# Performance work log

Measured on AMD Instinct MI355X. Metric: run time of the kernel, lower is better.

Reference implementation:

```python
import jax, jax.numpy as jnp
import numpy as np

N_USERS = 100_000
N_ITEMS = 50_000
N_NODES = N_USERS + N_ITEMS
D = 64
NUM_LAYERS = 3
N_INTER = 1_000_000  # interactions; symmetrized -> 2M directed edges
BATCH = 4096


def setup_inputs() -> dict:
    key = jax.random.key(0)
    k_u, k_i, k_r, k_c, k_uid, k_iid = jax.random.split(key, 6)
    user_embedding = jax.random.normal(k_u, (N_USERS, D), dtype=jnp.float32)
    item_embedding = jax.random.normal(k_i, (N_ITEMS, D), dtype=jnp.float32)

    # build symmetric normalized adjacency edges as in get_norm_adj_mat
    rng = np.random.default_rng(0)
    row = rng.integers(0, N_USERS, size=N_INTER)
    col = rng.integers(0, N_ITEMS, size=N_INTER) + N_USERS
    src = np.concatenate([row, col])
    dst = np.concatenate([col, row])
    deg = np.bincount(src, minlength=N_NODES).astype(np.float32)
    norm_deg = 1.0 / np.sqrt(np.where(deg == 0, 1.0, deg))
    edge_weight = (norm_deg[src] * norm_deg[dst]).astype(np.float32)
    edge_index = np.stack([src, dst]).astype(np.int64)

    user_id = jax.random.randint(k_uid, (BATCH,), 0, N_USERS)
    item_id = jax.random.randint(k_iid, (BATCH,), 0, N_ITEMS)
    return {
        "user_embedding": user_embedding,
        "item_embedding": item_embedding,
        "edge_weight": jnp.asarray(edge_weight),
        "edge_index": jnp.asarray(edge_index),
        "user_id": user_id,
        "item_id": item_id,
    }


def reference(user_embedding, item_embedding, edge_weight, edge_index, user_id, item_id):
    # ego embeddings: [N_NODES, D]
    x = jnp.concatenate([user_embedding, item_embedding], axis=0)
    src, dst = edge_index[0], edge_index[1]
    h = x
    acc = x  # running sum over layer outputs (incl. layer 0)
    for _ in range(NUM_LAYERS):
        # LightGCNConv: gather source, scale by edge weight, scatter-add to dest
        msg = h[src] * edge_weight[:, None]                       # [E, D]
        h = jax.ops.segment_sum(msg, dst, num_segments=N_NODES)   # [N, D]
        acc = acc + h
    final = acc / jnp.asarray(NUM_LAYERS + 1, dtype=x.dtype)      # mean over layers
    u_embed = final[:N_USERS][user_id]
    i_embed = final[N_USERS:][item_id]
    return (u_embed, i_embed)
```

## Files before the change

### kernel.cpp

```cpp
#include <hip/hip_runtime.h>

#define N_USERS 100000
#define N_NODES 150000
#define DIM 64
#define BATCH 4096
#define BSHIFT 8
#define BUCKET 256
#define NB 586
#define NBP 768
#define PAIRS_PER_BLK 2048
#define STRIP 4096
#define CAPSHIFT 13
#define CAP (1 << CAPSHIFT)

typedef unsigned short bf16_t;

static __device__ __forceinline__ float bf2f(bf16_t h) {
    return __uint_as_float(((unsigned)h) << 16);
}
static __device__ __forceinline__ bf16_t f2bf(float f) {
    unsigned u = __float_as_uint(f);
    return (bf16_t)((u + 0x7FFFu + ((u >> 16) & 1u)) >> 16);
}

__global__ void __launch_bounds__(256)
lgcn_bin(const int* __restrict__ row, const int* __restrict__ col,
         int* __restrict__ pos, int* __restrict__ binned, int EH) {
    __shared__ int cnt[NBP];
    __shared__ int sA[256], sB[256];
    __shared__ int base[NB + 2];
    __shared__ int stage[STRIP];
    int tid = threadIdx.x;
    int k = blockIdx.x;
    cnt[tid] = 0; cnt[tid + 256] = 0; cnt[tid + 512] = 0;
    __syncthreads();
    int e0 = k * PAIRS_PER_BLK;
    int e1 = min(EH, e0 + PAIRS_PER_BLK);
    int n = e1 - e0;
    int nq = n >> 2;
    const int4* r4 = (const int4*)(row + e0);
    const int4* c4 = (const int4*)(col + e0);
    for (int q = tid; q < nq; q += 256) {
        int4 r = r4[q]; int4 c = c4[q];
        atomicAdd(&cnt[r.x >> BSHIFT], 1); atomicAdd(&cnt[c.x >> BSHIFT], 1);
        atomicAdd(&cnt[r.y >> BSHIFT], 1); atomicAdd(&cnt[c.y >> BSHIFT], 1);
        atomicAdd(&cnt[r.z >> BSHIFT], 1); atomicAdd(&cnt[c.z >> BSHIFT], 1);
        atomicAdd(&cnt[r.w >> BSHIFT], 1); atomicAdd(&cnt[c.w >> BSHIFT], 1);
    }
    __syncthreads();
    int c0 = cnt[3 * tid], c1 = cnt[3 * tid + 1], c2 = cnt[3 * tid + 2];
    int s = c0 + c1 + c2;
    sA[tid] = s;
    __syncthreads();
    int* c_ = sA; int* n_ = sB;
    for (int off = 1; off < 256; off <<= 1) {
        n_[tid] = (tid >= off) ? c_[tid] + c_[tid - off] : c_[tid];
        __syncthreads();
        int* t = c_; c_ = n_; n_ = t;
    }
    int excl = c_[tid] - s;
    if (3 * tid     <= NB) base[3 * tid]     = excl;
    if (3 * tid + 1 <= NB) base[3 * tid + 1] = excl + c0;
    if (3 * tid + 2 <= NB) base[3 * tid + 2] = excl + c0 + c1;
    __syncthreads();
    for (int i = tid; i <= NB; i += 256) {
        pos[k * (NB + 1) + i] = base[i];
        cnt[i] = base[i];
    }
    __syncthreads();
    for (int q = tid; q < nq; q += 256) {
        int4 r = r4[q]; int4 c = c4[q];
        int rr[4] = { r.x, r.y, r.z, r.w };
        int cc[4] = { c.x, c.y, c.z, c.w };
#pragma unroll
        for (int j = 0; j < 4; ++j) {
            int p1 = atomicAdd(&cnt[cc[j] >> BSHIFT], 1);
            stage[p1] = ((cc[j] & (BUCKET - 1)) << 18) | rr[j];
            int p2 = atomicAdd(&cnt[rr[j] >> BSHIFT], 1);
            stage[p2] = ((rr[j] & (BUCKET - 1)) << 18) | cc[j];
        }
    }
    __syncthreads();
    int m4 = (2 * n) >> 2;
    int4* dst = (int4*)(binned + k * STRIP);
    const int4* st4 = (const int4*)stage;
    for (int j = tid; j < m4; j += 256) dst[j] = st4[j];
}

__global__ void __launch_bounds__(256)
lgcn_build_csr(const int* __restrict__ pos, const int* __restrict__ binned,
               int4* __restrict__ nodeinfo, int* __restrict__ packed,
               const float* __restrict__ ue, const float* __restrict__ ie,
               bf16_t* __restrict__ g0, bf16_t* __restrict__ g1, int nblk) {
    __shared__ int stage[CAP];
    __shared__ int sA[256], sB[256];
    __shared__ int hist[256], cur[256];
    int b = blockIdx.x;
    int tid = threadIdx.x;
    int gb = b << CAPSHIFT;
    int a0 = 0, l0 = 0, a1 = 0, l1 = 0;
    if (tid < nblk) {
        const int* pk = pos + tid * (NB + 1) + b;
        a0 = pk[0]; l0 = pk[1] - a0;
    }
    if (tid + 256 < nblk) {
        const int* pk = pos + (tid + 256) * (NB + 1) + b;
        a1 = pk[0]; l1 = pk[1] - a1;
    }
    int u = l0 + l1;
    sA[tid] = u;
    __syncthreads();
    int* c_ = sA; int* n_ = sB;
    for (int off = 1; off < 256; off <<= 1) {
        n_[tid] = (tid >= off) ? c_[tid] + c_[tid - off] : c_[tid];
        __syncthreads();
        int* t = c_; c_ = n_; n_ = t;
    }
    int myBase = c_[tid] - u;
    int Eb = c_[255];
    __syncthreads();
    {
        const int* s0 = binned + tid * STRIP + a0;
        int i = 0;
        for (; i + 4 <= l0; i += 4) {
            int w0 = s0[i], w1 = s0[i + 1], w2 = s0[i + 2], w3 = s0[i + 3];
            stage[myBase + i] = w0;     stage[myBase + i + 1] = w1;
            stage[myBase + i + 2] = w2; stage[myBase + i + 3] = w3;
        }
        for (; i < l0; ++i) stage[myBase + i] = s0[i];
        const int* s1 = binned + (tid + 256) * STRIP + a1;
        int bb = myBase + l0;
        i = 0;
        for (; i + 4 <= l1; i += 4) {
            int w0 = s1[i], w1 = s1[i + 1], w2 = s1[i + 2], w3 = s1[i + 3];
            stage[bb + i] = w0;     stage[bb + i + 1] = w1;
            stage[bb + i + 2] = w2; stage[bb + i + 3] = w3;
        }
        for (; i < l1; ++i) stage[bb + i] = s1[i];
    }
    hist[tid] = 0;
    __syncthreads();
    for (int j = tid; j < Eb; j += 256)
        atomicAdd(&hist[stage[j] >> 18], 1);
    __syncthreads();
    int deg = hist[tid];
    int degp = (deg + 3) & ~3;
    sA[tid] = degp;
    __syncthreads();
    int* c2 = sA; int* n2 = sB;
    for (int off = 1; off < 256; off <<= 1) {
        n2[tid] = (tid >= off) ? c2[tid] + c2[tid - off] : c2[tid];
        __syncthreads();
        int* t = c2; c2 = n2; n2 = t;
    }
    int startLoc = c2[tid] - degp;
    cur[tid] = startLoc;
    int node = (b << BSHIFT) + tid;
    float da = (deg == 0) ? 1.0f : (float)deg;
    float sq = sqrtf(da);
    float nm = 1.0f / sq;
    if (node < N_NODES) {
        int4 ni;
        ni.x = gb + startLoc;
        ni.y = deg;
        ni.z = __float_as_int(nm);
        ni.w = __float_as_int(sq);
        nodeinfo[node] = ni;
    }
    __syncthreads();
    hist[tid] = __float_as_int(nm);
    for (int kk = deg; kk < degp; ++kk)
        packed[gb + startLoc + kk] = N_NODES;
    for (int j = tid; j < Eb; j += 256) {
        int w = stage[j];
        int p = atomicAdd(&cur[w >> 18], 1);
        packed[gb + p] = w & 0x3FFFF;
    }
    int firstNode = b << BSHIFT;
    int nloc = min(BUCKET, N_NODES - firstNode);
    const int nU16 = N_USERS * (DIM / 4);
    int t0 = firstNode * (DIM / 4);
    for (int i = tid; i < nloc * (DIM / 4); i += 256) {
        int t = t0 + i;
        float4 x = (t < nU16) ? ((const float4*)ue)[t]
                              : ((const float4*)ie)[t - nU16];
        float nrm = __int_as_float(hist[i >> 4]);
        ushort4 o;
        o.x = f2bf(x.x * nrm); o.y = f2bf(x.y * nrm);
        o.z = f2bf(x.z * nrm); o.w = f2bf(x.w * nrm);
        ((ushort4*)g0)[t] = o;
    }
    if (b == 0 && tid < 32) {
        const int nT = N_NODES * (DIM / 4);
        if (tid < 16) ((ushort4*)g0)[nT + tid] = make_ushort4(0, 0, 0, 0);
        else          ((ushort4*)g1)[nT + tid - 16] = make_ushort4(0, 0, 0, 0);
    }
}


static __device__ __forceinline__ float
gather_lane(const bf16_t* __restrict__ g, const int* __restrict__ packed,
            int su, int dp, int lane) {
    float acc = 0.f;
    const int4* p4 = (const int4*)(packed + su);
    int k = 0;
    for (; k + 8 <= dp; k += 8) {
        int4 ea = p4[k >> 2];
        int4 eb = p4[(k >> 2) + 1];
        const bf16_t* r0 = g + ((unsigned)ea.x << 6);
        const bf16_t* r1 = g + ((unsigned)ea.y << 6);
        const bf16_t* r2 = g + ((unsigned)ea.z << 6);
        const bf16_t* r3 = g + ((unsigned)ea.w << 6);
        const bf16_t* r4 = g + ((unsigned)eb.x << 6);
        const bf16_t* r5 = g + ((unsigned)eb.y << 6);
        const bf16_t* r6 = g + ((unsigned)eb.z << 6);
        const bf16_t* r7 = g + ((unsigned)eb.w << 6);
        float v0 = bf2f(r0[lane]); float v1 = bf2f(r1[lane]);
        float v2 = bf2f(r2[lane]); float v3 = bf2f(r3[lane]);
        float v4 = bf2f(r4[lane]); float v5 = bf2f(r5[lane]);
        float v6 = bf2f(r6[lane]); float v7 = bf2f(r7[lane]);
        acc += ((v0 + v1) + (v2 + v3)) + ((v4 + v5) + (v6 + v7));
    }
    if (k < dp) {
        int4 ea = p4[k >> 2];
        const bf16_t* r0 = g + ((unsigned)ea.x << 6);
        const bf16_t* r1 = g + ((unsigned)ea.y << 6);
        const bf16_t* r2 = g + ((unsigned)ea.z << 6);
        const bf16_t* r3 = g + ((unsigned)ea.w << 6);
        float v0 = bf2f(r0[lane]); float v1 = bf2f(r1[lane]);
        float v2 = bf2f(r2[lane]); float v3 = bf2f(r3[lane]);
        acc += (v0 + v1) + (v2 + v3);
    }
    return acc;
}

__global__ void __launch_bounds__(256)
lgcn_pull(const bf16_t* __restrict__ g, const int4* __restrict__ nodeinfo,
          const int* __restrict__ packed, bf16_t* __restrict__ gn) {
    int n = blockIdx.x * 4 + (threadIdx.x >> 6);
    if (n >= N_NODES) return;
    n = __builtin_amdgcn_readfirstlane(n);
    int lane = threadIdx.x & 63;
    int4 ni = nodeinfo[n];
    int su = __builtin_amdgcn_readfirstlane(ni.x);
    int du = __builtin_amdgcn_readfirstlane(ni.y);
    int dp = (du + 3) & ~3;
    float acc = gather_lane(g, packed, su, dp, lane);
    float nm = __int_as_float(ni.z);
    gn[((unsigned)n << 6) + lane] = f2bf(acc * nm * nm);
}

__global__ void __launch_bounds__(256)
lgcn_final(const float* __restrict__ ue, const float* __restrict__ ie,
           const bf16_t* __restrict__ g1, const bf16_t* __restrict__ g2,
           const int4* __restrict__ nodeinfo, const int* __restrict__ packed,
           const int* __restrict__ uid, const int* __restrict__ iid,
           float* __restrict__ out) {
    int slot = blockIdx.x * 4 + (threadIdx.x >> 6);
    if (slot >= 2 * BATCH) return;
    slot = __builtin_amdgcn_readfirstlane(slot);
    int lane = threadIdx.x & 63;
    int isItem = slot >= BATCH;
    int b = isItem ? (slot - BATCH) : slot;
    int node = isItem ? (N_USERS + iid[b]) : uid[b];
    node = __builtin_amdgcn_readfirstlane(node);
    int4 ni = nodeinfo[node];
    int su = __builtin_amdgcn_readfirstlane(ni.x);
    int du = __builtin_amdgcn_readfirstlane(ni.y);
    int dp = (du + 3) & ~3;
    float acc = gather_lane(g2, packed, su, dp, lane);
    const float* xb = isItem ? (ie + ((unsigned)(node - N_USERS) << 6))
                             : (ue + ((unsigned)node << 6));
    float x = xb[lane];
    float a1 = bf2f(g1[((unsigned)node << 6) + lane]);
    float a2 = bf2f(g2[((unsigned)node << 6) + lane]);
    float rn = __int_as_float(ni.w);
    float nm = __int_as_float(ni.z);
    out[((unsigned)slot << 6) + lane] = 0.25f * (x + rn * (a1 + a2) + nm * acc);
}


extern "C" void kernel_launch(void* const* d_in, const int* in_sizes, int n_in,
                              void* d_out, int out_size, void* d_ws, size_t ws_size,
                              hipStream_t stream) {
    const float* ue  = (const float*)d_in[0];
    const float* ie  = (const float*)d_in[1];
    const int*   ei  = (const int*)d_in[3];
    const int*   uid = (const int*)d_in[4];
    const int*   iid = (const int*)d_in[5];
    float* out = (float*)d_out;

    const int E  = in_sizes[2];
    const int EH = E / 2;
    const int* row = ei;
    const int* col = ei + E;

    const int nblk = (EH + PAIRS_PER_BLK - 1) / PAIRS_PER_BLK;

    char* p = (char*)d_ws;
    size_t off = 0;
    auto carve = [&](size_t bytes) -> char* {
        char* r = p + off;
        off += (bytes + 255) & ~(size_t)255;
        return r;
    };
    const size_t nodeBf16 = (size_t)(N_NODES + 1) * DIM * sizeof(bf16_t);
    bf16_t* gA       = (bf16_t*)carve(nodeBf16);
    bf16_t* gB       = (bf16_t*)carve(nodeBf16);
    int4*   nodeinfo = (int4*)carve((size_t)N_NODES * sizeof(int4));
    int*    pos      = (int*)carve((size_t)nblk * (NB + 1) * sizeof(int));
    int*    binned   = (int*)carve((size_t)nblk * STRIP * sizeof(int));
    int*    packed   = (int*)carve((size_t)NB * CAP * sizeof(int));
    (void)ws_size;

    lgcn_bin<<<nblk, 256, 0, stream>>>(row, col, pos, binned, EH);
    lgcn_build_csr<<<NB, 256, 0, stream>>>(pos, binned, nodeinfo, packed,
                                           ue, ie, gA, gB, nblk);
    const int pullGrid = (N_NODES + 3) / 4;
    lgcn_pull<<<pullGrid, 256, 0, stream>>>(gA, nodeinfo, packed, gB);
    lgcn_pull<<<pullGrid, 256, 0, stream>>>(gB, nodeinfo, packed, gA);
    lgcn_final<<<(2 * BATCH + 3) / 4, 256, 0, stream>>>(
        ue, ie, gB, gA, nodeinfo, packed, uid, iid, out);
}
```

Baseline: 225.5 us.

## Fuse propagation layers and final gather into one persistent kernel with grid barriers

Replaces the two pull launches and the final kernel with a single persistent kernel of 2048 blocks. Waves grid-stride over nodes and are separated by atomic-counter grid barriers, and the counter is reset inside the bin kernel. This removes two kernel launch boundaries and their tail drain, at the cost of spin-wait barriers and a fixed grid that must be fully co-resident to avoid deadlock. Static node striding may also balance load worse than one wave per node.

```diff
diff --git a/kernel.cpp b/kernel.cpp
--- a/kernel.cpp
+++ b/kernel.cpp
@@ -12,6 +12,8 @@
 #define STRIP 4096
 #define CAPSHIFT 13
 #define CAP (1 << CAPSHIFT)
+#define PROP_BLOCKS 2048
+#define PROP_WAVES (PROP_BLOCKS * 4)
 
 typedef unsigned short bf16_t;
 
@@ -25,13 +27,15 @@
 
 __global__ void __launch_bounds__(256)
 lgcn_bin(const int* __restrict__ row, const int* __restrict__ col,
-         int* __restrict__ pos, int* __restrict__ binned, int EH) {
+         int* __restrict__ pos, int* __restrict__ binned, int EH,
+         int* __restrict__ bar) {
     __shared__ int cnt[NBP];
     __shared__ int sA[256], sB[256];
     __shared__ int base[NB + 2];
     __shared__ int stage[STRIP];
     int tid = threadIdx.x;
     int k = blockIdx.x;
+    if (k == 0 && tid == 0) bar[0] = 0;
     cnt[tid] = 0; cnt[tid + 256] = 0; cnt[tid + 512] = 0;
     __syncthreads();
     int e0 = k * PAIRS_PER_BLK;
@@ -234,49 +238,73 @@
     return acc;
 }
 
-__global__ void __launch_bounds__(256)
-lgcn_pull(const bf16_t* __restrict__ g, const int4* __restrict__ nodeinfo,
-          const int* __restrict__ packed, bf16_t* __restrict__ gn) {
-    int n = blockIdx.x * 4 + (threadIdx.x >> 6);
-    if (n >= N_NODES) return;
-    n = __builtin_amdgcn_readfirstlane(n);
+static __device__ __forceinline__ void
+grid_barrier(int* bar, int target) {
+    __syncthreads();
+    if (threadIdx.x == 0) {
+        __hip_atomic_fetch_add(bar, 1, __ATOMIC_RELEASE,
+                               __HIP_MEMORY_SCOPE_AGENT);
+        while (__hip_atomic_load(bar, __ATOMIC_RELAXED,
+                                 __HIP_MEMORY_SCOPE_AGENT) < target)
+            __builtin_amdgcn_s_sleep(64);
+        (void)__hip_atomic_load(bar, __ATOMIC_ACQUIRE,
+                                __HIP_MEMORY_SCOPE_AGENT);
+    }
+    __syncthreads();
+}
+
+__global__ void __launch_bounds__(256, 8)
+lgcn_prop(bf16_t* __restrict__ gA, bf16_t* __restrict__ gB,
+          const int4* __restrict__ nodeinfo, const int* __restrict__ packed,
+          const float* __restrict__ ue, const float* __restrict__ ie,
+          const int* __restrict__ uid, const int* __restrict__ iid,
+          float* __restrict__ out, int* bar) {
+    int gw = blockIdx.x * 4 + (threadIdx.x >> 6);
     int lane = threadIdx.x & 63;
-    int4 ni = nodeinfo[n];
-    int su = __builtin_amdgcn_readfirstlane(ni.x);
-    int du = __builtin_amdgcn_readfirstlane(ni.y);
-    int dp = (du + 3) & ~3;
-    float acc = gather_lane(g, packed, su, dp, lane);
-    float nm = __int_as_float(ni.z);
-    gn[((unsigned)n << 6) + lane] = f2bf(acc * nm * nm);
-}
-
-__global__ void __launch_bounds__(256)
-lgcn_final(const float* __restrict__ ue, const float* __restrict__ ie,
-           const bf16_t* __restrict__ g1, const bf16_t* __restrict__ g2,
-           const int4* __restrict__ nodeinfo, const int* __restrict__ packed,
-           const int* __restrict__ uid, const int* __restrict__ iid,
-           float* __restrict__ out) {
-    int slot = blockIdx.x * 4 + (threadIdx.x >> 6);
-    if (slot >= 2 * BATCH) return;
-    slot = __builtin_amdgcn_readfirstlane(slot);
-    int lane = threadIdx.x & 63;
-    int isItem = slot >= BATCH;
-    int b = isItem ? (slot - BATCH) : slot;
-    int node = isItem ? (N_USERS + iid[b]) : uid[b];
-    node = __builtin_amdgcn_readfirstlane(node);
-    int4 ni = nodeinfo[node];
-    int su = __builtin_amdgcn_readfirstlane(ni.x);
-    int du = __builtin_amdgcn_readfirstlane(ni.y);
-    int dp = (du + 3) & ~3;
-    float acc = gather_lane(g2, packed, su, dp, lane);
-    const float* xb = isItem ? (ie + ((unsigned)(node - N_USERS) << 6))
-                             : (ue + ((unsigned)node << 6));
-    float x = xb[lane];
-    float a1 = bf2f(g1[((unsigned)node << 6) + lane]);
-    float a2 = bf2f(g2[((unsigned)node << 6) + lane]);
-    float rn = __int_as_float(ni.w);
-    float nm = __int_as_float(ni.z);
-    out[((unsigned)slot << 6) + lane] = 0.25f * (x + rn * (a1 + a2) + nm * acc);
+    for (int n0 = gw; n0 < N_NODES; n0 += PROP_WAVES) {
+        int n = __builtin_amdgcn_readfirstlane(n0);
+        int4 ni = nodeinfo[n];
+        int su = __builtin_amdgcn_readfirstlane(ni.x);
+        int du = __builtin_amdgcn_readfirstlane(ni.y);
+        int dp = (du + 3) & ~3;
+        float acc = gather_lane(gA, packed, su, dp, lane);
+        float nm = __int_as_float(ni.z);
+        gB[((unsigned)n << 6) + lane] = f2bf(acc * nm * nm);
+    }
+    grid_barrier(bar, PROP_BLOCKS);
+    for (int n0 = gw; n0 < N_NODES; n0 += PROP_WAVES) {
+        int n = __builtin_amdgcn_readfirstlane(n0);
+        int4 ni = nodeinfo[n];
+        int su = __builtin_amdgcn_readfirstlane(ni.x);
+        int du = __builtin_amdgcn_readfirstlane(ni.y);
+        int dp = (du + 3) & ~3;
+        float acc = gather_lane(gB, packed, su, dp, lane);
+        float nm = __int_as_float(ni.z);
+        gA[((unsigned)n << 6) + lane] = f2bf(acc * nm * nm);
+    }
+    grid_barrier(bar, 2 * PROP_BLOCKS);
+    int slot = gw;
+    if (slot < 2 * BATCH) {
+        slot = __builtin_amdgcn_readfirstlane(slot);
+        int isItem = slot >= BATCH;
+        int b = isItem ? (slot - BATCH) : slot;
+        int node = isItem ? (N_USERS + iid[b]) : uid[b];
+        node = __builtin_amdgcn_readfirstlane(node);
+        int4 ni = nodeinfo[node];
+        int su = __builtin_amdgcn_readfirstlane(ni.x);
+        int du = __builtin_amdgcn_readfirstlane(ni.y);
+        int dp = (du + 3) & ~3;
+        float acc = gather_lane(gA, packed, su, dp, lane);
+        const float* xb = isItem ? (ie + ((unsigned)(node - N_USERS) << 6))
+                                 : (ue + ((unsigned)node << 6));
+        float x = xb[lane];
+        float a1 = bf2f(gB[((unsigned)node << 6) + lane]);
+        float a2 = bf2f(gA[((unsigned)node << 6) + lane]);
+        float rn = __int_as_float(ni.w);
+        float nm = __int_as_float(ni.z);
+        out[((unsigned)slot << 6) + lane] =
+            0.25f * (x + rn * (a1 + a2) + nm * acc);
+    }
 }
 
 
@@ -311,14 +339,12 @@
     int*    pos      = (int*)carve((size_t)nblk * (NB + 1) * sizeof(int));
     int*    binned   = (int*)carve((size_t)nblk * STRIP * sizeof(int));
     int*    packed   = (int*)carve((size_t)NB * CAP * sizeof(int));
+    int*    bar      = (int*)carve(256);
     (void)ws_size;
 
-    lgcn_bin<<<nblk, 256, 0, stream>>>(row, col, pos, binned, EH);
+    lgcn_bin<<<nblk, 256, 0, stream>>>(row, col, pos, binned, EH, bar);
     lgcn_build_csr<<<NB, 256, 0, stream>>>(pos, binned, nodeinfo, packed,
                                            ue, ie, gA, gB, nblk);
-    const int pullGrid = (N_NODES + 3) / 4;
-    lgcn_pull<<<pullGrid, 256, 0, stream>>>(gA, nodeinfo, packed, gB);
-    lgcn_pull<<<pullGrid, 256, 0, stream>>>(gB, nodeinfo, packed, gA);
-    lgcn_final<<<(2 * BATCH + 3) / 4, 256, 0, stream>>>(
-        ue, ie, gB, gA, nodeinfo, packed, uid, iid, out);
-}
+    lgcn_prop<<<PROP_BLOCKS, 256, 0, stream>>>(gA, gB, nodeinfo, packed,
+                                               ue, ie, uid, iid, out, bar);
+}
```

After: 623.4 us. 177% more time.
